# Kernel optimization log

Hardware: AMD Instinct MI355X
Metric: run time of the kernel (lower is better)

Reference implementation:

```python
import jax, jax.numpy as jnp
import numpy as np

NEG_SLOPE = 0.01  # torch nn.LeakyReLU default

def _lrelu(x):
    return jnp.where(x >= 0, x, NEG_SLOPE * x)

def setup_inputs() -> dict:
    key = jax.random.key(0)
    ks = jax.random.split(key, 10)
    B, Din, C = 128, 2048, 2048
    H = C // 2            # 1024
    OUT, KD = C // 4, 20  # 512, 20 (MBD)
    s = lambda k, shape, fan: jax.random.normal(k, shape, jnp.float32) / np.sqrt(fan)
    return {
        "inputs": jax.random.normal(ks[0], (B, Din), jnp.float32),
        "W1": s(ks[1], (Din, C), Din), "b1": jnp.zeros((C,), jnp.float32),
        "W2": s(ks[2], (C, H), C),     "b2": jnp.zeros((H,), jnp.float32),
        "W3": s(ks[3], (H, H), H),     "b3": jnp.zeros((H,), jnp.float32),
        "T":  jax.random.normal(ks[4], (H, OUT, KD), jnp.float32),
        "Wc": s(ks[5], (H + OUT, 1), H + OUT), "bc": jnp.zeros((1,), jnp.float32),
    }

def reference(inputs, W1, b1, W2, b2, W3, b3, T, Wc, bc):
    # dense stack: Linear + LeakyReLU x3
    h = _lrelu(inputs @ W1 + b1)          # [B, 2048]
    h = _lrelu(h @ W2 + b2)               # [B, 1024]
    h = _lrelu(h @ W3 + b3)               # [B, 1024]
    # minibatch discrimination
    Hd, OUT, KD = T.shape
    M = (h @ T.reshape(Hd, OUT * KD)).reshape(-1, OUT, KD)   # [B, OUT, KD]
    # pairwise L1 over kernel dim: [B, B, OUT]
    norm = jnp.abs(M[None, :, :, :] - M[:, None, :, :]).sum(-1)
    o_b = jnp.exp(-norm).sum(0) - 1.0     # [B, OUT] (subtract self-term)
    feat = jnp.concatenate([h, o_b], axis=1)  # [B, 1536]
    return feat @ Wc + bc                 # [B, 1]
```

## Files before the change

### kernel.cpp

```cpp
#include <hip/hip_runtime.h>
#include <hip/hip_bf16.h>


typedef __bf16 bf16x8 __attribute__((ext_vector_type(8)));
typedef float  f32x4  __attribute__((ext_vector_type(4)));

static __device__ __forceinline__ unsigned int f2bf(float f) {
  union { float f; unsigned int u; } v; v.f = f;
  unsigned int r = v.u + 0x7FFFu + ((v.u >> 16) & 1u);
  return r >> 16;
}

static __device__ __forceinline__ float lrelu(float x) {
  return x >= 0.0f ? x : 0.01f * x;
}

static __device__ __forceinline__ void fma4(float4& c, float a, const float4& w) {
  c.x = fmaf(a, w.x, c.x); c.y = fmaf(a, w.y, c.y);
  c.z = fmaf(a, w.z, c.z); c.w = fmaf(a, w.w, c.w);
}

__global__ __launch_bounds__(256, 2) void gemm_f32(
    const float* __restrict__ A, const float* __restrict__ W,
    float* __restrict__ P, int lda, int N, int kchunk)
{
  __shared__ __align__(16) float As[16 * 128];
  __shared__ __align__(16) float Ws[16 * 32];
  const int t     = threadIdx.x;
  const int c0    = blockIdx.x * 32;
  const int kbase = blockIdx.y * kchunk;
  const int rowg  = t >> 3;
  const int colg  = t & 7;

  float4 acc[4];
  acc[0] = make_float4(0, 0, 0, 0); acc[1] = make_float4(0, 0, 0, 0);
  acc[2] = make_float4(0, 0, 0, 0); acc[3] = make_float4(0, 0, 0, 0);

  for (int kt = 0; kt < kchunk; kt += 16) {
    const int k0 = kbase + kt;
    {
      int r = t >> 1, kh = (t & 1) * 8;
      const float* ap = A + (size_t)r * lda + k0 + kh;
      float4 a0 = *(const float4*)ap;
      float4 a1 = *(const float4*)(ap + 4);
      As[(kh + 0) * 128 + r] = a0.x; As[(kh + 1) * 128 + r] = a0.y;
      As[(kh + 2) * 128 + r] = a0.z; As[(kh + 3) * 128 + r] = a0.w;
      As[(kh + 4) * 128 + r] = a1.x; As[(kh + 5) * 128 + r] = a1.y;
      As[(kh + 6) * 128 + r] = a1.z; As[(kh + 7) * 128 + r] = a1.w;
    }
    {
      int kw = t >> 4, f = t & 15;
      float2 w = *(const float2*)(W + (size_t)(k0 + kw) * N + c0 + f * 2);
      *(float2*)(Ws + kw * 32 + f * 2) = w;
    }
    __syncthreads();
    #pragma unroll
    for (int k = 0; k < 16; k++) {
      float4 w = *(const float4*)(Ws + k * 32 + colg * 4);
      float4 a = *(const float4*)(As + k * 128 + rowg * 4);
      fma4(acc[0], a.x, w); fma4(acc[1], a.y, w);
      fma4(acc[2], a.z, w); fma4(acc[3], a.w, w);
    }
    __syncthreads();
  }

  float* op = P + (size_t)blockIdx.y * 128 * N + (size_t)(rowg * 4) * N + c0 + colg * 4;
  *(float4*)op            = acc[0];
  *(float4*)(op + N)      = acc[1];
  *(float4*)(op + 2 * N)  = acc[2];
  *(float4*)(op + 3 * N)  = acc[3];
}

__global__ __launch_bounds__(256) void reduce_ep(
    const float* __restrict__ P, const float* __restrict__ bias,
    float* __restrict__ outF, unsigned short* __restrict__ outB,
    int N, int S, int ldo)
{
  const int gid = blockIdx.x * 256 + threadIdx.x;
  const int c4  = N >> 2;
  const int r   = gid / c4;
  const int c   = (gid - r * c4) * 4;
  float4 s = make_float4(0, 0, 0, 0);
  for (int si = 0; si < S; si++) {
    float4 p = *(const float4*)(P + (size_t)si * 128 * N + (size_t)r * N + c);
    s.x += p.x; s.y += p.y; s.z += p.z; s.w += p.w;
  }
  float4 b = *(const float4*)(bias + c);
  s.x = lrelu(s.x + b.x); s.y = lrelu(s.y + b.y);
  s.z = lrelu(s.z + b.z); s.w = lrelu(s.w + b.w);
  *(float4*)(outF + (size_t)r * ldo + c) = s;
  if (outB) {
    ushort4 u;
    u.x = (unsigned short)f2bf(s.x); u.y = (unsigned short)f2bf(s.y);
    u.z = (unsigned short)f2bf(s.z); u.w = (unsigned short)f2bf(s.w);
    *(ushort4*)(outB + (size_t)r * N + c) = u;
  }
}

__global__ __launch_bounds__(256, 2) void gemm4_mfma(
    const unsigned short* __restrict__ h3b, const float* __restrict__ T,
    float* __restrict__ accM)
{
  __shared__ __align__(16) unsigned short Asm[128 * 32];
  __shared__ __align__(16) unsigned int   Wst[64 * 20];
  const int t     = threadIdx.x;
  const int c0    = blockIdx.x * 64;
  const int kbase = blockIdx.y * 512;
  const int lane  = t & 63, wave = t >> 6;
  const int ml    = lane & 15, q = lane >> 4;
  const int r0    = wave * 32;

  f32x4 acc[2][4];
  #pragma unroll
  for (int i = 0; i < 2; i++)
    #pragma unroll
    for (int j = 0; j < 4; j++) acc[i][j] = (f32x4){0.f, 0.f, 0.f, 0.f};

  for (int kt = 0; kt < 16; kt++) {
    const int k0 = kbase + kt * 32;
    {
      int r = t >> 2, qq = t & 3;
      uint4 v0 = *(const uint4*)(h3b + (size_t)r * 1024 + k0 + qq * 8);
      uint4 v1 = *(const uint4*)(h3b + (size_t)(r + 64) * 1024 + k0 + qq * 8);
      *(uint4*)(Asm + r * 32 + qq * 8)        = v0;
      *(uint4*)(Asm + (r + 64) * 32 + qq * 8) = v1;
    }
    {
      int kp = t >> 4, n4 = (t & 15) * 4;
      const float* w0 = T + (size_t)(k0 + 2 * kp) * 10240 + c0 + n4;
      float4 wa = *(const float4*)w0;
      float4 wb = *(const float4*)(w0 + 10240);
      Wst[(n4 + 0) * 20 + kp] = f2bf(wa.x) | (f2bf(wb.x) << 16);
      Wst[(n4 + 1) * 20 + kp] = f2bf(wa.y) | (f2bf(wb.y) << 16);
      Wst[(n4 + 2) * 20 + kp] = f2bf(wa.z) | (f2bf(wb.z) << 16);
      Wst[(n4 + 3) * 20 + kp] = f2bf(wa.w) | (f2bf(wb.w) << 16);
    }
    __syncthreads();
    bf16x8 a0 = *(const bf16x8*)(Asm + (r0 + ml) * 32 + q * 8);
    bf16x8 a1 = *(const bf16x8*)(Asm + (r0 + 16 + ml) * 32 + q * 8);
    #pragma unroll
    for (int ct = 0; ct < 4; ct++) {
      bf16x8 b = *(const bf16x8*)((const unsigned short*)Wst +
                                  (size_t)((ct * 16 + ml) * 20 + q * 4) * 2);
      acc[0][ct] = __builtin_amdgcn_mfma_f32_16x16x32_bf16(a0, b, acc[0][ct], 0, 0, 0);
      acc[1][ct] = __builtin_amdgcn_mfma_f32_16x16x32_bf16(a1, b, acc[1][ct], 0, 0, 0);
    }
    __syncthreads();
  }

  float* out = accM + (size_t)blockIdx.y * 128 * 10240;
  #pragma unroll
  for (int rt = 0; rt < 2; rt++)
    #pragma unroll
    for (int ct = 0; ct < 4; ct++) {
      int col = c0 + ct * 16 + ml;
      int row = r0 + rt * 16 + q * 4;
      #pragma unroll
      for (int i = 0; i < 4; i++)
        out[(size_t)(row + i) * 10240 + col] = acc[rt][ct][i];
    }
}

__global__ __launch_bounds__(256) void pairwise(
    const float* __restrict__ accM, float* __restrict__ feat)
{
  __shared__ __align__(16) float Ml[128 * 20];
  __shared__ float parts[8 * 128];
  const int t = threadIdx.x;
  const int o = blockIdx.x;
  {
    int i = t >> 1, kh = (t & 1) * 10;
    const float* p0 = accM + (size_t)i * 10240 + o * 20 + kh;
    const float* p1 = p0 + (size_t)128 * 10240;
    #pragma unroll
    for (int k = 0; k < 10; k++) Ml[i * 20 + kh + k] = p0[k] + p1[k];
  }
  __syncthreads();

  const int jg = t & 31, ihalf = t >> 5;
  float mj[4][20];
  #pragma unroll
  for (int c = 0; c < 4; c++) {
    const float* src = Ml + (size_t)(jg * 4 + c) * 20;
    #pragma unroll
    for (int k = 0; k < 20; k++) mj[c][k] = src[k];
  }
  float acc[4] = {0.f, 0.f, 0.f, 0.f};
  for (int ii = 0; ii < 16; ii++) {
    int i = ihalf * 16 + ii;
    const float4* m4 = (const float4*)(Ml + (size_t)i * 20);
    float mi[20];
    *(float4*)(mi + 0)  = m4[0]; *(float4*)(mi + 4)  = m4[1];
    *(float4*)(mi + 8)  = m4[2]; *(float4*)(mi + 12) = m4[3];
    *(float4*)(mi + 16) = m4[4];
    #pragma unroll
    for (int c = 0; c < 4; c++) {
      float norm = 0.f;
      #pragma unroll
      for (int k = 0; k < 20; k++) norm += fabsf(mi[k] - mj[c][k]);
      acc[c] += __expf(-norm);
    }
  }
  #pragma unroll
  for (int c = 0; c < 4; c++) parts[ihalf * 128 + jg * 4 + c] = acc[c];
  __syncthreads();
  if (t < 128) {
    float s = 0.f;
    #pragma unroll
    for (int ih = 0; ih < 8; ih++) s += parts[ih * 128 + t];
    feat[(size_t)t * 1536 + 1024 + o] = s - 1.0f;
  }
}

__global__ __launch_bounds__(256) void final_dot(
    const float* __restrict__ feat, const float* __restrict__ Wc,
    const float* __restrict__ bc, float* __restrict__ out)
{
  __shared__ float red[4];
  const int t = threadIdx.x, r = blockIdx.x;
  float s = 0.f;
  for (int c = t; c < 1536; c += 256) s += feat[(size_t)r * 1536 + c] * Wc[c];
  for (int off = 32; off > 0; off >>= 1) s += __shfl_down(s, off);
  if ((t & 63) == 0) red[t >> 6] = s;
  __syncthreads();
  if (t == 0) out[r] = red[0] + red[1] + red[2] + red[3] + bc[0];
}

extern "C" void kernel_launch(void* const* d_in, const int* in_sizes, int n_in,
                              void* d_out, int out_size, void* d_ws, size_t ws_size,
                              hipStream_t stream)
{
  const float* X  = (const float*)d_in[0];
  const float* W1 = (const float*)d_in[1];
  const float* b1 = (const float*)d_in[2];
  const float* W2 = (const float*)d_in[3];
  const float* b2 = (const float*)d_in[4];
  const float* W3 = (const float*)d_in[5];
  const float* b3 = (const float*)d_in[6];
  const float* T  = (const float*)d_in[7];
  const float* Wc = (const float*)d_in[8];
  const float* bc = (const float*)d_in[9];

  char* ws = (char*)d_ws;
  float*          P    = (float*)ws;
  float*          accM = (float*)ws;
  float*          h1   = (float*)(ws + 10485760);
  float*          h2   = (float*)(ws + 11534336);
  unsigned short* h3b  = (unsigned short*)(ws + 12058624);
  float*          feat = (float*)(ws + 12320768);
  float*          out  = (float*)d_out;

  gemm_f32<<<dim3(64, 8), 256, 0, stream>>>(X, W1, P, 2048, 2048, 256);
  reduce_ep<<<256, 256, 0, stream>>>(P, b1, h1, nullptr, 2048, 8, 2048);
  gemm_f32<<<dim3(32, 16), 256, 0, stream>>>(h1, W2, P, 2048, 1024, 128);
  reduce_ep<<<128, 256, 0, stream>>>(P, b2, h2, nullptr, 1024, 16, 1024);
  gemm_f32<<<dim3(32, 8), 256, 0, stream>>>(h2, W3, P, 1024, 1024, 128);
  reduce_ep<<<128, 256, 0, stream>>>(P, b3, feat, h3b, 1024, 8, 1536);
  gemm4_mfma<<<dim3(160, 2), 256, 0, stream>>>(h3b, T, accM);
  pairwise<<<512, 256, 0, stream>>>(accM, feat);
  final_dot<<<128, 256, 0, stream>>>(feat, Wc, bc, out);
}
```

Before: 207.1 us.

## Prefetch GEMM tiles into registers, store MBD partials as bf16, retune launches

The fp32 GEMM and the MFMA GEMM now load the next K-tile into registers while the current tile is being computed, overlapping global loads with math. The MFMA GEMM uses four K-splits instead of two, pads the A shared tile, and writes its partial results as bf16 to halve write and read traffic; the pairwise kernel sums the four bf16 partials. Pairwise uses 512 threads with two columns per thread, reduce_ep uses 128-thread blocks, and the launch-bound occupancy hints rise to 4. Rounding the partial sums to bf16 adds error to M, and that error is amplified by exp(-L1).

```diff
diff --git a/kernel.cpp b/kernel.cpp
--- a/kernel.cpp
+++ b/kernel.cpp
@@ -10,17 +10,19 @@
   unsigned int r = v.u + 0x7FFFu + ((v.u >> 16) & 1u);
   return r >> 16;
 }
-
+static __device__ __forceinline__ float bf2f(unsigned short u) {
+  union { unsigned int u; float f; } v; v.u = ((unsigned int)u) << 16;
+  return v.f;
+}
 static __device__ __forceinline__ float lrelu(float x) {
   return x >= 0.0f ? x : 0.01f * x;
 }
-
 static __device__ __forceinline__ void fma4(float4& c, float a, const float4& w) {
   c.x = fmaf(a, w.x, c.x); c.y = fmaf(a, w.y, c.y);
   c.z = fmaf(a, w.z, c.z); c.w = fmaf(a, w.w, c.w);
 }
 
-__global__ __launch_bounds__(256, 2) void gemm_f32(
+__global__ __launch_bounds__(256, 4) void gemm_f32(
     const float* __restrict__ A, const float* __restrict__ W,
     float* __restrict__ P, int lda, int N, int kchunk)
 {
@@ -31,29 +33,33 @@
   const int kbase = blockIdx.y * kchunk;
   const int rowg  = t >> 3;
   const int colg  = t & 7;
+  const int r_s   = t >> 1, kh_s = (t & 1) * 8;
+  const int kw_s  = t >> 4, f_s  = (t & 15) * 2;
 
   float4 acc[4];
   acc[0] = make_float4(0, 0, 0, 0); acc[1] = make_float4(0, 0, 0, 0);
   acc[2] = make_float4(0, 0, 0, 0); acc[3] = make_float4(0, 0, 0, 0);
 
+  const float* aptr = A + (size_t)r_s * lda + kbase + kh_s;
+  const float* wptr = W + (size_t)(kbase + kw_s) * N + c0 + f_s;
+  float4 pa0 = *(const float4*)aptr;
+  float4 pa1 = *(const float4*)(aptr + 4);
+  float2 pw  = *(const float2*)wptr;
+
   for (int kt = 0; kt < kchunk; kt += 16) {
-    const int k0 = kbase + kt;
-    {
-      int r = t >> 1, kh = (t & 1) * 8;
-      const float* ap = A + (size_t)r * lda + k0 + kh;
-      float4 a0 = *(const float4*)ap;
-      float4 a1 = *(const float4*)(ap + 4);
-      As[(kh + 0) * 128 + r] = a0.x; As[(kh + 1) * 128 + r] = a0.y;
-      As[(kh + 2) * 128 + r] = a0.z; As[(kh + 3) * 128 + r] = a0.w;
-      As[(kh + 4) * 128 + r] = a1.x; As[(kh + 5) * 128 + r] = a1.y;
-      As[(kh + 6) * 128 + r] = a1.z; As[(kh + 7) * 128 + r] = a1.w;
-    }
-    {
-      int kw = t >> 4, f = t & 15;
-      float2 w = *(const float2*)(W + (size_t)(k0 + kw) * N + c0 + f * 2);
-      *(float2*)(Ws + kw * 32 + f * 2) = w;
-    }
-    __syncthreads();
+    As[(kh_s + 0) * 128 + r_s] = pa0.x; As[(kh_s + 1) * 128 + r_s] = pa0.y;
+    As[(kh_s + 2) * 128 + r_s] = pa0.z; As[(kh_s + 3) * 128 + r_s] = pa0.w;
+    As[(kh_s + 4) * 128 + r_s] = pa1.x; As[(kh_s + 5) * 128 + r_s] = pa1.y;
+    As[(kh_s + 6) * 128 + r_s] = pa1.z; As[(kh_s + 7) * 128 + r_s] = pa1.w;
+    *(float2*)(Ws + kw_s * 32 + f_s) = pw;
+    __syncthreads();
+    if (kt + 16 < kchunk) {
+      aptr += 16;
+      wptr += (size_t)16 * N;
+      pa0 = *(const float4*)aptr;
+      pa1 = *(const float4*)(aptr + 4);
+      pw  = *(const float2*)wptr;
+    }
     #pragma unroll
     for (int k = 0; k < 16; k++) {
       float4 w = *(const float4*)(Ws + k * 32 + colg * 4);
@@ -65,18 +71,18 @@
   }
 
   float* op = P + (size_t)blockIdx.y * 128 * N + (size_t)(rowg * 4) * N + c0 + colg * 4;
-  *(float4*)op            = acc[0];
-  *(float4*)(op + N)      = acc[1];
-  *(float4*)(op + 2 * N)  = acc[2];
-  *(float4*)(op + 3 * N)  = acc[3];
-}
-
-__global__ __launch_bounds__(256) void reduce_ep(
+  *(float4*)op           = acc[0];
+  *(float4*)(op + N)     = acc[1];
+  *(float4*)(op + 2 * N) = acc[2];
+  *(float4*)(op + 3 * N) = acc[3];
+}
+
+__global__ __launch_bounds__(128) void reduce_ep(
     const float* __restrict__ P, const float* __restrict__ bias,
     float* __restrict__ outF, unsigned short* __restrict__ outB,
     int N, int S, int ldo)
 {
-  const int gid = blockIdx.x * 256 + threadIdx.x;
+  const int gid = blockIdx.x * 128 + threadIdx.x;
   const int c4  = N >> 2;
   const int r   = gid / c4;
   const int c   = (gid - r * c4) * 4;
@@ -97,18 +103,20 @@
   }
 }
 
-__global__ __launch_bounds__(256, 2) void gemm4_mfma(
+__global__ __launch_bounds__(256, 4) void gemm4_mfma(
     const unsigned short* __restrict__ h3b, const float* __restrict__ T,
-    float* __restrict__ accM)
-{
-  __shared__ __align__(16) unsigned short Asm[128 * 32];
+    unsigned short* __restrict__ accM)
+{
+  __shared__ __align__(16) unsigned short Asm[128 * 40];
   __shared__ __align__(16) unsigned int   Wst[64 * 20];
   const int t     = threadIdx.x;
   const int c0    = blockIdx.x * 64;
-  const int kbase = blockIdx.y * 512;
+  const int kbase = blockIdx.y * 256;
   const int lane  = t & 63, wave = t >> 6;
   const int ml    = lane & 15, q = lane >> 4;
   const int r0    = wave * 32;
+  const int ra = t >> 2, qa = t & 3;
+  const int kp = t & 15, n4 = (t >> 4) * 4;
 
   f32x4 acc[2][4];
   #pragma unroll
@@ -116,28 +124,31 @@
     #pragma unroll
     for (int j = 0; j < 4; j++) acc[i][j] = (f32x4){0.f, 0.f, 0.f, 0.f};
 
-  for (int kt = 0; kt < 16; kt++) {
-    const int k0 = kbase + kt * 32;
-    {
-      int r = t >> 2, qq = t & 3;
-      uint4 v0 = *(const uint4*)(h3b + (size_t)r * 1024 + k0 + qq * 8);
-      uint4 v1 = *(const uint4*)(h3b + (size_t)(r + 64) * 1024 + k0 + qq * 8);
-      *(uint4*)(Asm + r * 32 + qq * 8)        = v0;
-      *(uint4*)(Asm + (r + 64) * 32 + qq * 8) = v1;
-    }
-    {
-      int kp = t >> 4, n4 = (t & 15) * 4;
-      const float* w0 = T + (size_t)(k0 + 2 * kp) * 10240 + c0 + n4;
-      float4 wa = *(const float4*)w0;
-      float4 wb = *(const float4*)(w0 + 10240);
-      Wst[(n4 + 0) * 20 + kp] = f2bf(wa.x) | (f2bf(wb.x) << 16);
-      Wst[(n4 + 1) * 20 + kp] = f2bf(wa.y) | (f2bf(wb.y) << 16);
-      Wst[(n4 + 2) * 20 + kp] = f2bf(wa.z) | (f2bf(wb.z) << 16);
-      Wst[(n4 + 3) * 20 + kp] = f2bf(wa.w) | (f2bf(wb.w) << 16);
-    }
-    __syncthreads();
-    bf16x8 a0 = *(const bf16x8*)(Asm + (r0 + ml) * 32 + q * 8);
-    bf16x8 a1 = *(const bf16x8*)(Asm + (r0 + 16 + ml) * 32 + q * 8);
+  const unsigned short* ap = h3b + (size_t)ra * 1024 + kbase + qa * 8;
+  const float*          tp = T + (size_t)(kbase + 2 * kp) * 10240 + c0 + n4;
+  uint4  va0 = *(const uint4*)ap;
+  uint4  va1 = *(const uint4*)(ap + 64 * 1024);
+  float4 vw0 = *(const float4*)tp;
+  float4 vw1 = *(const float4*)(tp + 10240);
+
+  for (int kt = 0; kt < 8; kt++) {
+    *(uint4*)(Asm + ra * 40 + qa * 8)        = va0;
+    *(uint4*)(Asm + (ra + 64) * 40 + qa * 8) = va1;
+    Wst[(n4 + 0) * 20 + kp] = f2bf(vw0.x) | (f2bf(vw1.x) << 16);
+    Wst[(n4 + 1) * 20 + kp] = f2bf(vw0.y) | (f2bf(vw1.y) << 16);
+    Wst[(n4 + 2) * 20 + kp] = f2bf(vw0.z) | (f2bf(vw1.z) << 16);
+    Wst[(n4 + 3) * 20 + kp] = f2bf(vw0.w) | (f2bf(vw1.w) << 16);
+    __syncthreads();
+    if (kt < 7) {
+      ap += 32;
+      tp += (size_t)32 * 10240;
+      va0 = *(const uint4*)ap;
+      va1 = *(const uint4*)(ap + 64 * 1024);
+      vw0 = *(const float4*)tp;
+      vw1 = *(const float4*)(tp + 10240);
+    }
+    bf16x8 a0 = *(const bf16x8*)(Asm + (r0 + ml) * 40 + q * 8);
+    bf16x8 a1 = *(const bf16x8*)(Asm + (r0 + 16 + ml) * 40 + q * 8);
     #pragma unroll
     for (int ct = 0; ct < 4; ct++) {
       bf16x8 b = *(const bf16x8*)((const unsigned short*)Wst +
@@ -148,7 +159,7 @@
     __syncthreads();
   }
 
-  float* out = accM + (size_t)blockIdx.y * 128 * 10240;
+  unsigned short* out = accM + (size_t)blockIdx.y * 128 * 10240;
   #pragma unroll
   for (int rt = 0; rt < 2; rt++)
     #pragma unroll
@@ -157,35 +168,38 @@
       int row = r0 + rt * 16 + q * 4;
       #pragma unroll
       for (int i = 0; i < 4; i++)
-        out[(size_t)(row + i) * 10240 + col] = acc[rt][ct][i];
-    }
-}
-
-__global__ __launch_bounds__(256) void pairwise(
-    const float* __restrict__ accM, float* __restrict__ feat)
+        out[(size_t)(row + i) * 10240 + col] = (unsigned short)f2bf(acc[rt][ct][i]);
+    }
+}
+
+__global__ __launch_bounds__(512, 4) void pairwise(
+    const unsigned short* __restrict__ accM, float* __restrict__ feat)
 {
   __shared__ __align__(16) float Ml[128 * 20];
   __shared__ float parts[8 * 128];
   const int t = threadIdx.x;
   const int o = blockIdx.x;
   {
-    int i = t >> 1, kh = (t & 1) * 10;
-    const float* p0 = accM + (size_t)i * 10240 + o * 20 + kh;
-    const float* p1 = p0 + (size_t)128 * 10240;
-    #pragma unroll
-    for (int k = 0; k < 10; k++) Ml[i * 20 + kh + k] = p0[k] + p1[k];
+    int i = t >> 2, kh = (t & 3) * 5;
+    const unsigned short* p = accM + (size_t)i * 10240 + o * 20 + kh;
+    #pragma unroll
+    for (int k = 0; k < 5; k++) {
+      float s = bf2f(p[k]) + bf2f(p[1310720 + k]) +
+                bf2f(p[2621440 + k]) + bf2f(p[3932160 + k]);
+      Ml[i * 20 + kh + k] = s;
+    }
   }
   __syncthreads();
 
-  const int jg = t & 31, ihalf = t >> 5;
-  float mj[4][20];
-  #pragma unroll
-  for (int c = 0; c < 4; c++) {
-    const float* src = Ml + (size_t)(jg * 4 + c) * 20;
+  const int jg = t & 63, ihalf = t >> 6;
+  float mj[2][20];
+  #pragma unroll
+  for (int c = 0; c < 2; c++) {
+    const float* src = Ml + (size_t)(jg * 2 + c) * 20;
     #pragma unroll
     for (int k = 0; k < 20; k++) mj[c][k] = src[k];
   }
-  float acc[4] = {0.f, 0.f, 0.f, 0.f};
+  float acc[2] = {0.f, 0.f};
   for (int ii = 0; ii < 16; ii++) {
     int i = ihalf * 16 + ii;
     const float4* m4 = (const float4*)(Ml + (size_t)i * 20);
@@ -194,7 +208,7 @@
     *(float4*)(mi + 8)  = m4[2]; *(float4*)(mi + 12) = m4[3];
     *(float4*)(mi + 16) = m4[4];
     #pragma unroll
-    for (int c = 0; c < 4; c++) {
+    for (int c = 0; c < 2; c++) {
       float norm = 0.f;
       #pragma unroll
       for (int k = 0; k < 20; k++) norm += fabsf(mi[k] - mj[c][k]);
@@ -202,7 +216,7 @@
     }
   }
   #pragma unroll
-  for (int c = 0; c < 4; c++) parts[ihalf * 128 + jg * 4 + c] = acc[c];
+  for (int c = 0; c < 2; c++) parts[ihalf * 128 + jg * 2 + c] = acc[c];
   __syncthreads();
   if (t < 128) {
     float s = 0.f;
@@ -243,7 +257,7 @@
 
   char* ws = (char*)d_ws;
   float*          P    = (float*)ws;
-  float*          accM = (float*)ws;
+  unsigned short* accB = (unsigned short*)ws;
   float*          h1   = (float*)(ws + 10485760);
   float*          h2   = (float*)(ws + 11534336);
   unsigned short* h3b  = (unsigned short*)(ws + 12058624);
@@ -251,12 +265,12 @@
   float*          out  = (float*)d_out;
 
   gemm_f32<<<dim3(64, 8), 256, 0, stream>>>(X, W1, P, 2048, 2048, 256);
-  reduce_ep<<<256, 256, 0, stream>>>(P, b1, h1, nullptr, 2048, 8, 2048);
+  reduce_ep<<<512, 128, 0, stream>>>(P, b1, h1, nullptr, 2048, 8, 2048);
   gemm_f32<<<dim3(32, 16), 256, 0, stream>>>(h1, W2, P, 2048, 1024, 128);
-  reduce_ep<<<128, 256, 0, stream>>>(P, b2, h2, nullptr, 1024, 16, 1024);
+  reduce_ep<<<256, 128, 0, stream>>>(P, b2, h2, nullptr, 1024, 16, 1024);
   gemm_f32<<<dim3(32, 8), 256, 0, stream>>>(h2, W3, P, 1024, 1024, 128);
-  reduce_ep<<<128, 256, 0, stream>>>(P, b3, feat, h3b, 1024, 8, 1536);
-  gemm4_mfma<<<dim3(160, 2), 256, 0, stream>>>(h3b, T, accM);
-  pairwise<<<512, 256, 0, stream>>>(accM, feat);
+  reduce_ep<<<256, 128, 0, stream>>>(P, b3, feat, h3b, 1024, 8, 1536);
+  gemm4_mfma<<<dim3(160, 4), 256, 0, stream>>>(h3b, T, accB);
+  pairwise<<<512, 512, 0, stream>>>(accB, feat);
   final_dot<<<128, 256, 0, stream>>>(feat, Wc, bc, out);
 }
```

Measured after the change: 193.5 us. -6.6%, faster.
